# Kernel optimization log

Hardware: AMD Instinct MI355X
Metric: run time of the kernel (lower is better)

The kernel has to match this reference:

```python
import math
import jax, jax.numpy as jnp
import numpy as np

N_STEPS = 5
STEP = 0.1      # step_size buffer (eval mode: never updated)
LMBD = 0.1
MU = 0.0
N_DICT = 1


def _prox(c):
    # elasnet_prox: softshrink(c * s_mu, lmbd*step * s_mu); with mu=0, s_mu=1
    s_mu = 1.0 / (1.0 + MU * STEP)
    lam = LMBD * STEP * s_mu
    c = c * s_mu
    return jnp.sign(c) * jnp.maximum(jnp.abs(c) - lam, 0.0)


def _fista(x, W):
    # x: [N, C], W: [D, C]; F.linear(x, W) == x @ W.T
    s = STEP
    # i == 0
    c = jax.nn.relu(_prox(s * (x @ W.T)))
    # i == 1
    c_pre = c
    r = x - c @ W                      # residual [N, C]
    c = jax.nn.relu(_prox(c + s * (r @ W.T)))
    t = (math.sqrt(5.0) + 1.0) / 2.0
    # i >= 2: FISTA momentum, gradient evaluated at c (as in source)
    for _ in range(2, N_STEPS):
        t_pre = t
        t = (math.sqrt(1.0 + 4.0 * t_pre * t_pre) + 1.0) / 2.0
        a = (t_pre + t - 1.0) / t * c + (1.0 - t_pre) / t * c_pre
        c_pre = c
        r = x - c @ W
        c = jax.nn.relu(_prox(a + s * (r @ W.T)))
    return c


def setup_inputs() -> dict:
    key = jax.random.key(0)
    k1, k2 = jax.random.split(key)
    x = jax.random.normal(k1, (8, 2048, 512), dtype=jnp.float32)
    # kaiming-uniform-like dictionary [dict_size, n_channel]
    bound = math.sqrt(6.0 / 512.0)
    weight = jax.random.uniform(k2, (2048, 512), dtype=jnp.float32,
                                minval=-bound, maxval=bound)
    return {"x": x, "weight": weight}


def reference(x, weight):
    bs, tok, dim = x.shape
    xf = x.reshape(-1, dim)                    # [N, C]
    c = _fista(xf, weight)                     # [N, D]
    xp = c @ weight                            # [N, C]
    r = xf - xp
    r_loss = jnp.sum(r * r) / N_DICT
    c_loss = LMBD * jnp.sum(jnp.abs(c)) + 0.5 * MU * jnp.sum(c * c)
    return (c.reshape(bs, tok, -1), xp.reshape(bs, tok, -1), r, r_loss, c_loss)
```

## Files before the change

### kernel.cpp

```cpp
#include <hip/hip_runtime.h>
#include <cmath>


typedef __attribute__((ext_vector_type(8))) short bf16x8;
typedef __attribute__((ext_vector_type(8))) unsigned short u16x8;
typedef __attribute__((ext_vector_type(4))) float f32x4;

constexpr float S_STEP = 0.1f;
constexpr float LAM    = 0.01f;

__device__ __forceinline__ unsigned short f2bf(float f) {
    unsigned u = __float_as_uint(f);
    u += 0x7FFFu + ((u >> 16) & 1u);
    return (unsigned short)(u >> 16);
}
__device__ __forceinline__ float bf2f(unsigned short s) {
    return __uint_as_float(((unsigned)s) << 16);
}

__device__ __forceinline__ void async16(const void* g, void* l) {
    __builtin_amdgcn_global_load_lds(
        (const __attribute__((address_space(1))) void*)g,
        (__attribute__((address_space(3))) void*)l, 16, 0, 0);
}

template<int EPI>
__global__ __launch_bounds__(256)
void gemm_bt(const short* __restrict__ A, const short* __restrict__ B,
             int K, int Nn,
             const unsigned short* Cc, const unsigned short* Cpre,
             const unsigned short* __restrict__ Xb,
             unsigned short* OutB, float* Out32,
             float cfA, float cfB, float* loss)
{
    __shared__ __align__(16) unsigned char smem[32768];
    short* S  = (short*)smem;
    float (*L)[132] = (float (*)[132])smem;
    float* red2 = (float*)(smem + 32736);

    const int tid  = threadIdx.x;
    const int wave = tid >> 6;
    const int lane = tid & 63;
    const int rowBase = blockIdx.y * 128;
    const int colBase = blockIdx.x * 128;

    const int sRow = lane >> 2;
    const int sK   = (lane & 3) << 3;
    const short* gA = A + (size_t)(rowBase + wave * 32 + sRow) * K + sK;
    const short* gB = B + (size_t)(colBase + wave * 32 + sRow) * K + sK;
    const size_t rstep = (size_t)16 * K;
    short* lA = S + (wave * 32) * 32;
    short* lB = S + 8192 + (wave * 32) * 32;

    const int m16  = lane & 15;
    const int quad = lane >> 4;
    const short* paBase = S + ((wave & 1) * 64 + m16) * 32 + quad * 8;
    const short* pbBase = S + 8192 + ((wave >> 1) * 64 + m16) * 32 + quad * 8;

    f32x4 acc[4][4] = {};
    const int nIter = K >> 5;

    {
        async16(gA,         lA);
        async16(gA + rstep, lA + 512);
        async16(gB,         lB);
        async16(gB + rstep, lB + 512);
    }

    for (int it = 0; it < nIter; ++it) {
        __syncthreads();
        if (it + 1 < nIter) {
            const int nb = (it + 1) & 1;
            const int kb = (it + 1) << 5;
            async16(gA + kb,         lA + nb * 4096);
            async16(gA + kb + rstep, lA + nb * 4096 + 512);
            async16(gB + kb,         lB + nb * 4096);
            async16(gB + kb + rstep, lB + nb * 4096 + 512);
        }
        const int cb = (it & 1) * 4096;
        bf16x8 af[4], bfr[4];
        #pragma unroll
        for (int i = 0; i < 4; ++i) af[i]  = *(const bf16x8*)(paBase + cb + i * 512);
        #pragma unroll
        for (int j = 0; j < 4; ++j) bfr[j] = *(const bf16x8*)(pbBase + cb + j * 512);
        #pragma unroll
        for (int i = 0; i < 4; ++i)
            #pragma unroll
            for (int j = 0; j < 4; ++j)
                acc[i][j] = __builtin_amdgcn_mfma_f32_16x16x32_bf16(
                                af[i], bfr[j], acc[i][j], 0, 0, 0);
    }

    const int lrow = tid >> 3;
    const int seg  = tid & 7;
    float lsum = 0.f;

    #pragma unroll
    for (int t = 0; t < 4; ++t) {
        __syncthreads();
        if ((wave & 1) == (t >> 1)) {
            #pragma unroll
            for (int ii = 0; ii < 2; ++ii) {
                const int i   = (t & 1) * 2 + ii;
                const int lr0 = ii * 16 + quad * 4;
                #pragma unroll
                for (int r = 0; r < 4; ++r)
                    #pragma unroll
                    for (int j = 0; j < 4; ++j)
                        L[lr0 + r][(wave >> 1) * 64 + j * 16 + m16] = acc[i][j][r];
            }
        }
        __syncthreads();

        float v[16];
        #pragma unroll
        for (int q = 0; q < 4; ++q)
            *(f32x4*)&v[q * 4] = *(const f32x4*)&L[lrow][seg * 16 + q * 4];

        const size_t gidx = (size_t)(rowBase + t * 32 + lrow) * Nn
                          + colBase + seg * 16;

        if constexpr (EPI == 0) {
            u16x8 o0, o1;
            #pragma unroll
            for (int k = 0; k < 8; ++k) {
                o0[k] = f2bf(fmaxf(S_STEP * v[k]     - LAM, 0.f));
                o1[k] = f2bf(fmaxf(S_STEP * v[k + 8] - LAM, 0.f));
            }
            *(u16x8*)(OutB + gidx)     = o0;
            *(u16x8*)(OutB + gidx + 8) = o1;
        } else if constexpr (EPI == 1 || EPI == 2) {
            const u16x8 cc0 = *(const u16x8*)(Cc   + gidx);
            const u16x8 cc1 = *(const u16x8*)(Cc   + gidx + 8);
            const u16x8 cp0 = *(const u16x8*)(Cpre + gidx);
            const u16x8 cp1 = *(const u16x8*)(Cpre + gidx + 8);
            float w[16];
            #pragma unroll
            for (int k = 0; k < 8; ++k) {
                w[k]     = fmaxf(cfA * bf2f(cc0[k]) + cfB * bf2f(cp0[k])
                                 + S_STEP * v[k]     - LAM, 0.f);
                w[k + 8] = fmaxf(cfA * bf2f(cc1[k]) + cfB * bf2f(cp1[k])
                                 + S_STEP * v[k + 8] - LAM, 0.f);
            }
            u16x8 o0, o1;
            #pragma unroll
            for (int k = 0; k < 8; ++k) { o0[k] = f2bf(w[k]); o1[k] = f2bf(w[k + 8]); }
            *(u16x8*)(OutB + gidx)     = o0;
            *(u16x8*)(OutB + gidx + 8) = o1;
            if constexpr (EPI == 2) {
                #pragma unroll
                for (int q = 0; q < 4; ++q)
                    *(f32x4*)(Out32 + gidx + q * 4) = *(const f32x4*)&w[q * 4];
                #pragma unroll
                for (int k = 0; k < 16; ++k) lsum += w[k];
            }
        } else if constexpr (EPI == 3) {
            const u16x8 xb0 = *(const u16x8*)(Xb + gidx);
            const u16x8 xb1 = *(const u16x8*)(Xb + gidx + 8);
            u16x8 o0, o1;
            #pragma unroll
            for (int k = 0; k < 8; ++k) {
                o0[k] = f2bf(bf2f(xb0[k]) - v[k]);
                o1[k] = f2bf(bf2f(xb1[k]) - v[k + 8]);
            }
            *(u16x8*)(OutB + gidx)     = o0;
            *(u16x8*)(OutB + gidx + 8) = o1;
        } else {
            #pragma unroll
            for (int q = 0; q < 4; ++q)
                *(f32x4*)(Out32 + gidx + q * 4) = *(const f32x4*)&v[q * 4];
        }
    }

    if constexpr (EPI == 2) {
        #pragma unroll
        for (int off = 32; off; off >>= 1) lsum += __shfl_down(lsum, off, 64);
        if (lane == 0) red2[wave] = lsum;
        __syncthreads();
        if (tid == 0)
            atomicAdd(loss, 0.1f * (red2[0] + red2[1] + red2[2] + red2[3]));
    }
}

__global__ __launch_bounds__(256)
void cvt_w_k(const float* __restrict__ W,
             unsigned short* __restrict__ Wb, unsigned short* __restrict__ Wtb)
{
    __shared__ unsigned short T[64][65];
    const int dBase = blockIdx.y * 64;
    const int cBase = blockIdx.x * 64;
    const int lc = threadIdx.x & 63;
    const int lr = threadIdx.x >> 6;
    #pragma unroll
    for (int p = 0; p < 16; ++p) {
        const int dl = p * 4 + lr;
        const size_t idx = (size_t)(dBase + dl) * 512 + cBase + lc;
        const unsigned short b = f2bf(W[idx]);
        Wb[idx] = b;
        T[dl][lc] = b;
    }
    __syncthreads();
    #pragma unroll
    for (int p = 0; p < 16; ++p) {
        const int cl = p * 4 + lr;
        Wtb[(size_t)(cBase + cl) * 2048 + dBase + lc] = T[lc][cl];
    }
}

__global__ __launch_bounds__(256)
void cvt_x_k(const float4* __restrict__ x4, ushort4* __restrict__ xb4, int n4)
{
    for (int i = blockIdx.x * 256 + threadIdx.x; i < n4; i += gridDim.x * 256) {
        const float4 v = x4[i];
        xb4[i] = make_ushort4(f2bf(v.x), f2bf(v.y), f2bf(v.z), f2bf(v.w));
    }
}

__global__ __launch_bounds__(256)
void finalize_k(const float4* __restrict__ x4, const float4* __restrict__ xp4,
                float4* __restrict__ r4, float* __restrict__ rloss, int n4)
{
    float lsum = 0.f;
    for (int i = blockIdx.x * 256 + threadIdx.x; i < n4; i += gridDim.x * 256) {
        const float4 xv = x4[i], pv = xp4[i];
        float4 rv;
        rv.x = xv.x - pv.x; rv.y = xv.y - pv.y;
        rv.z = xv.z - pv.z; rv.w = xv.w - pv.w;
        r4[i] = rv;
        lsum += rv.x * rv.x + rv.y * rv.y + rv.z * rv.z + rv.w * rv.w;
    }
    #pragma unroll
    for (int off = 32; off; off >>= 1) lsum += __shfl_down(lsum, off, 64);
    if ((threadIdx.x & 63) == 0) atomicAdd(rloss, lsum);
}

extern "C" void kernel_launch(void* const* d_in, const int* in_sizes, int n_in,
                              void* d_out, int out_size, void* d_ws, size_t ws_size,
                              hipStream_t stream)
{
    (void)in_sizes; (void)n_in; (void)out_size; (void)ws_size;

    constexpr int N = 16384, C = 512, D = 2048;
    constexpr size_t ND = (size_t)N * D;
    constexpr size_t NC = (size_t)N * C;

    const float* x = (const float*)d_in[0];
    const float* W = (const float*)d_in[1];

    float* out    = (float*)d_out;
    float* c_out  = out;
    float* xp_out = out + ND;
    float* r_out  = out + ND + NC;
    float* rloss  = out + ND + 2 * NC;
    float* closs  = rloss + 1;

    short* cb0 = (short*)d_ws;
    short* cb1 = cb0 + ND;

    unsigned short* rb  = (unsigned short*)xp_out;
    unsigned short* Wb  = (unsigned short*)xp_out + NC;
    unsigned short* Wtb = (unsigned short*)r_out;
    unsigned short* xb  = (unsigned short*)r_out + (size_t)D * C;

    hipMemsetAsync((void*)rloss, 0, 2 * sizeof(float), stream);

    double tp = (std::sqrt(5.0) + 1.0) / 2.0;
    float cfA[5] = {0.f, 1.f, 0.f, 0.f, 0.f};
    float cfB[5] = {0.f, 0.f, 0.f, 0.f, 0.f};
    for (int i = 2; i < 5; ++i) {
        double t = (std::sqrt(1.0 + 4.0 * tp * tp) + 1.0) / 2.0;
        cfA[i] = (float)((tp + t - 1.0) / t);
        cfB[i] = (float)((1.0 - tp) / t);
        tp = t;
    }

    const dim3 blk(256);
    cvt_w_k<<<dim3(C / 64, D / 64), blk, 0, stream>>>(W, Wb, Wtb);
    cvt_x_k<<<dim3(1024), blk, 0, stream>>>((const float4*)x, (ushort4*)xb,
                                            (int)(NC / 4));

    const dim3 gridD(D / 128, N / 128);
    const dim3 gridC(C / 128, N / 128);

    gemm_bt<0><<<gridD, blk, 0, stream>>>((const short*)xb, (const short*)Wb,
                                          C, D, nullptr, nullptr, nullptr,
                                          (unsigned short*)cb0, nullptr,
                                          0.f, 0.f, nullptr);

    short* bufs[2] = {cb0, cb1};
    for (int i = 1; i < 5; ++i) {
        const short* cprev = bufs[(i - 1) & 1];
        short*       cnew  = bufs[i & 1];
        const unsigned short* cpre2 =
            (i == 1) ? (const unsigned short*)cprev : (const unsigned short*)cnew;
        gemm_bt<3><<<gridC, blk, 0, stream>>>(cprev, (const short*)Wtb,
                                              D, C, nullptr, nullptr, xb,
                                              rb, nullptr, 0.f, 0.f, nullptr);
        if (i < 4)
            gemm_bt<1><<<gridD, blk, 0, stream>>>((const short*)rb, (const short*)Wb,
                                                  C, D, (const unsigned short*)cprev,
                                                  cpre2, nullptr,
                                                  (unsigned short*)cnew, nullptr,
                                                  cfA[i], cfB[i], nullptr);
        else
            gemm_bt<2><<<gridD, blk, 0, stream>>>((const short*)rb, (const short*)Wb,
                                                  C, D, (const unsigned short*)cprev,
                                                  cpre2, nullptr,
                                                  (unsigned short*)cnew, c_out,
                                                  cfA[i], cfB[i], closs);
    }

    gemm_bt<4><<<gridC, blk, 0, stream>>>(cb0, (const short*)Wtb,
                                          D, C, nullptr, nullptr, nullptr,
                                          nullptr, xp_out, 0.f, 0.f, nullptr);

    finalize_k<<<dim3(1024), blk, 0, stream>>>((const float4*)x,
                                               (const float4*)xp_out,
                                               (float4*)r_out, rloss,
                                               (int)(NC / 4));
}
```

Baseline: 833.7 us.

## Use 256x256-tile, 512-thread, 4-stage pipelined GEMM for the dictionary-projection kernels

Adds a specialized gemm256 kernel for the N×D projections (K=512, D=2048). It uses 256x256 output tiles, 8 waves, a 4-deep async global-to-LDS ring with XOR swizzle, and interleaved loads with MFMA under setprio. It also swizzles the block index for L2 locality. Larger tiles raise arithmetic intensity and cut repeated reads of A/B. The cost is 128KB of LDS per block, which limits occupancy, and only 512 blocks in the grid.

```diff
diff --git a/kernel.cpp b/kernel.cpp
--- a/kernel.cpp
+++ b/kernel.cpp
@@ -22,6 +22,186 @@
     __builtin_amdgcn_global_load_lds(
         (const __attribute__((address_space(1))) void*)g,
         (__attribute__((address_space(3))) void*)l, 16, 0, 0);
+}
+
+template<int EPI>
+__global__ __launch_bounds__(512, 2)
+void gemm256(const short* __restrict__ A, const short* __restrict__ B,
+             const unsigned short* __restrict__ Cc,
+             const unsigned short* __restrict__ Cpre,
+             unsigned short* __restrict__ OutB, float* __restrict__ Out32,
+             float cfA, float cfB, float* __restrict__ loss)
+{
+    constexpr int K = 512, Nn = 2048, NT = 16;
+    __shared__ __align__(16) unsigned char smem[131072];
+    short* S  = (short*)smem;
+    float* Lf = (float*)smem;
+    float* red = (float*)(smem + 131072 - 64);
+
+    const int tid  = threadIdx.x;
+    const int wave = tid >> 6;
+    const int lane = tid & 63;
+    const int wr   = wave >> 2;
+    const int wc   = wave & 3;
+    const int m16  = lane & 15;
+    const int quad = lane >> 4;
+
+    const int swz = (blockIdx.x & 7) * 64 + (blockIdx.x >> 3);
+    const int bx  = swz & 7;
+    const int by  = swz >> 3;
+    const int rowBase = by * 256, colBase = bx * 256;
+
+    const int s0 = wave * 64 + lane, s1 = s0 + 512;
+    const short* gA0 = A + (size_t)(rowBase + (s0 >> 2)) * K + ((s0 & 3) ^ ((s0 >> 3) & 3)) * 8;
+    const short* gA1 = A + (size_t)(rowBase + (s1 >> 2)) * K + ((s1 & 3) ^ ((s1 >> 3) & 3)) * 8;
+    const short* gB0 = B + (size_t)(colBase + (s0 >> 2)) * K + ((s0 & 3) ^ ((s0 >> 3) & 3)) * 8;
+    const short* gB1 = B + (size_t)(colBase + (s1 >> 2)) * K + ((s1 & 3) ^ ((s1 >> 3) & 3)) * 8;
+
+    const int dA0 = wave * 1024;
+    const int dA1 = 8192  + wave * 1024;
+    const int dB0 = 16384 + wave * 1024;
+    const int dB1 = 24576 + wave * 1024;
+
+    const int kcp   = quad ^ ((m16 >> 1) & 3);
+    const int aOffE = (wr * 128 + m16) * 32 + kcp * 8;
+    const int bOffE = 8192 + (wc * 64 + m16) * 32 + kcp * 8;
+
+    #pragma unroll
+    for (int tp = 0; tp < 3; ++tp) {
+        unsigned char* sb = smem + tp * 32768;
+        async16(gA0 + tp * 32, sb + dA0);
+        async16(gA1 + tp * 32, sb + dA1);
+        async16(gB0 + tp * 32, sb + dB0);
+        async16(gB1 + tp * 32, sb + dB1);
+    }
+    asm volatile("s_waitcnt vmcnt(8)" ::: "memory");
+    __builtin_amdgcn_s_barrier();
+
+    f32x4 acc[8][4] = {};
+    bf16x8 af[8], bfr[4];
+
+    for (int t = 0; t < NT; ++t) {
+        const short* Sl = S + (t & 3) * 16384;
+        unsigned char* stb = smem + ((t + 3) & 3) * 32768;
+        const bool st = (t + 3 < NT);
+
+        #pragma unroll
+        for (int i = 0; i < 4; ++i) af[i]  = *(const bf16x8*)(Sl + aOffE + i * 512);
+        #pragma unroll
+        for (int j = 0; j < 4; ++j) bfr[j] = *(const bf16x8*)(Sl + bOffE + j * 512);
+        if (st) {
+            async16(gA0 + (t + 3) * 32, stb + dA0);
+            async16(gA1 + (t + 3) * 32, stb + dA1);
+        }
+        __builtin_amdgcn_s_barrier();
+        __builtin_amdgcn_s_setprio(1);
+        #pragma unroll
+        for (int i = 0; i < 4; ++i)
+            #pragma unroll
+            for (int j = 0; j < 4; ++j)
+                acc[i][j] = __builtin_amdgcn_mfma_f32_16x16x32_bf16(
+                                af[i], bfr[j], acc[i][j], 0, 0, 0);
+        __builtin_amdgcn_s_setprio(0);
+        __builtin_amdgcn_s_barrier();
+
+        #pragma unroll
+        for (int i = 4; i < 8; ++i) af[i] = *(const bf16x8*)(Sl + aOffE + i * 512);
+        if (st) {
+            async16(gB0 + (t + 3) * 32, stb + dB0);
+            async16(gB1 + (t + 3) * 32, stb + dB1);
+        }
+        __builtin_amdgcn_s_barrier();
+        __builtin_amdgcn_s_setprio(1);
+        #pragma unroll
+        for (int i = 4; i < 8; ++i)
+            #pragma unroll
+            for (int j = 0; j < 4; ++j)
+                acc[i][j] = __builtin_amdgcn_mfma_f32_16x16x32_bf16(
+                                af[i], bfr[j], acc[i][j], 0, 0, 0);
+        __builtin_amdgcn_s_setprio(0);
+        if (t <= NT - 4)      asm volatile("s_waitcnt vmcnt(8)" ::: "memory");
+        else if (t == NT - 3) asm volatile("s_waitcnt vmcnt(4)" ::: "memory");
+        else if (t <  NT - 1) asm volatile("s_waitcnt vmcnt(0)" ::: "memory");
+        __builtin_amdgcn_s_barrier();
+    }
+
+    const int row_l = tid >> 3;
+    const int seg   = tid & 7;
+    const bool useCp = (cfB != 0.f);
+    float lsum = 0.f;
+
+    #pragma unroll
+    for (int c = 0; c < 4; ++c) {
+        __syncthreads();
+        if (wr == (c >> 1)) {
+            #pragma unroll
+            for (int ii = 0; ii < 4; ++ii) {
+                const int i = (c & 1) * 4 + ii;
+                #pragma unroll
+                for (int j = 0; j < 4; ++j)
+                    #pragma unroll
+                    for (int r = 0; r < 4; ++r)
+                        Lf[(ii * 16 + quad * 4 + r) * 260 + wc * 64 + j * 16 + m16]
+                            = acc[i][j][r];
+            }
+        }
+        __syncthreads();
+
+        float v[32];
+        #pragma unroll
+        for (int q = 0; q < 8; ++q)
+            *(f32x4*)&v[q * 4] = *(const f32x4*)&Lf[row_l * 260 + seg * 32 + q * 4];
+
+        const size_t gidx = (size_t)(rowBase + c * 64 + row_l) * Nn
+                          + colBase + seg * 32;
+
+        if constexpr (EPI == 0) {
+            #pragma unroll
+            for (int h = 0; h < 4; ++h) {
+                u16x8 o;
+                #pragma unroll
+                for (int k = 0; k < 8; ++k)
+                    o[k] = f2bf(fmaxf(S_STEP * v[h * 8 + k] - LAM, 0.f));
+                *(u16x8*)(OutB + gidx + h * 8) = o;
+            }
+        } else {
+            float w[32];
+            #pragma unroll
+            for (int h = 0; h < 4; ++h) {
+                const u16x8 cc = *(const u16x8*)(Cc + gidx + h * 8);
+                u16x8 cp = {};
+                if (useCp) cp = *(const u16x8*)(Cpre + gidx + h * 8);
+                u16x8 o;
+                #pragma unroll
+                for (int k = 0; k < 8; ++k) {
+                    w[h * 8 + k] = fmaxf(cfA * bf2f(cc[k]) + cfB * bf2f(cp[k])
+                                         + S_STEP * v[h * 8 + k] - LAM, 0.f);
+                    o[k] = f2bf(w[h * 8 + k]);
+                }
+                *(u16x8*)(OutB + gidx + h * 8) = o;
+            }
+            if constexpr (EPI == 2) {
+                #pragma unroll
+                for (int q = 0; q < 8; ++q)
+                    *(f32x4*)(Out32 + gidx + q * 4) = *(const f32x4*)&w[q * 4];
+                #pragma unroll
+                for (int k = 0; k < 32; ++k) lsum += w[k];
+            }
+        }
+    }
+
+    if constexpr (EPI == 2) {
+        #pragma unroll
+        for (int off = 32; off; off >>= 1) lsum += __shfl_down(lsum, off, 64);
+        if (lane == 0) red[wave] = lsum;
+        __syncthreads();
+        if (tid == 0) {
+            float s = 0.f;
+            #pragma unroll
+            for (int wv = 0; wv < 8; ++wv) s += red[wv];
+            atomicAdd(loss, 0.1f * s);
+        }
+    }
 }
 
 template<int EPI>
@@ -279,13 +459,13 @@
     cvt_x_k<<<dim3(1024), blk, 0, stream>>>((const float4*)x, (ushort4*)xb,
                                             (int)(NC / 4));
 
-    const dim3 gridD(D / 128, N / 128);
+    const dim3 gridD256(512);
+    const dim3 blk512(512);
     const dim3 gridC(C / 128, N / 128);
 
-    gemm_bt<0><<<gridD, blk, 0, stream>>>((const short*)xb, (const short*)Wb,
-                                          C, D, nullptr, nullptr, nullptr,
-                                          (unsigned short*)cb0, nullptr,
-                                          0.f, 0.f, nullptr);
+    gemm256<0><<<gridD256, blk512, 0, stream>>>(
+        (const short*)xb, (const short*)Wb, nullptr, nullptr,
+        (unsigned short*)cb0, nullptr, 0.f, 0.f, nullptr);
 
     short* bufs[2] = {cb0, cb1};
     for (int i = 1; i < 5; ++i) {
@@ -297,17 +477,15 @@
                                               D, C, nullptr, nullptr, xb,
                                               rb, nullptr, 0.f, 0.f, nullptr);
         if (i < 4)
-            gemm_bt<1><<<gridD, blk, 0, stream>>>((const short*)rb, (const short*)Wb,
-                                                  C, D, (const unsigned short*)cprev,
-                                                  cpre2, nullptr,
-                                                  (unsigned short*)cnew, nullptr,
-                                                  cfA[i], cfB[i], nullptr);
+            gemm256<1><<<gridD256, blk512, 0, stream>>>(
+                (const short*)rb, (const short*)Wb,
+                (const unsigned short*)cprev, cpre2,
+                (unsigned short*)cnew, nullptr, cfA[i], cfB[i], nullptr);
         else
-            gemm_bt<2><<<gridD, blk, 0, stream>>>((const short*)rb, (const short*)Wb,
-                                                  C, D, (const unsigned short*)cprev,
-                                                  cpre2, nullptr,
-                                                  (unsigned short*)cnew, c_out,
-                                                  cfA[i], cfB[i], closs);
+            gemm256<2><<<gridD256, blk512, 0, stream>>>(
+                (const short*)rb, (const short*)Wb,
+                (const unsigned short*)cprev, cpre2,
+                (unsigned short*)cnew, c_out, cfA[i], cfB[i], closs);
     }
 
     gemm_bt<4><<<gridC, blk, 0, stream>>>(cb0, (const short*)Wtb,
```

Result: slower. 924.2 us (+10.9%).
